# Kernel optimization log

Measured on AMD Instinct MI355X. Metric: run time of the kernel, lower is better.

## Reference

```python
import jax, jax.numpy as jnp
import numpy as np

KERNEL_MUL = 2.0
KERNEL_NUM = 5


def _mmd(source, target, kernel_mul=KERNEL_MUL, kernel_num=KERNEL_NUM, fix_sigma=None):
    n = source.shape[0]
    total = jnp.concatenate([source, target], axis=0)  # [2N, D]
    n_samples = total.shape[0]
    # Pairwise squared L2 distances via Gram matrix (same math as the
    # broadcasted (2N,2N,D) diff-square-sum, but O(N^2 D) GEMM instead).
    sq = jnp.sum(total * total, axis=1)                # [2N]
    gram = total @ total.T                             # [2N, 2N]
    L2 = sq[:, None] + sq[None, :] - 2.0 * gram        # [2N, 2N]
    if fix_sigma:
        bandwidth = fix_sigma
    else:
        # torch used L2_distance.data -> detached; match with stop_gradient
        bandwidth = jax.lax.stop_gradient(jnp.sum(L2)) / (n_samples ** 2 - n_samples)
    bandwidth = bandwidth / (kernel_mul ** (kernel_num // 2))
    kernels = jnp.zeros_like(L2)
    for i in range(kernel_num):
        kernels = kernels + jnp.exp(-L2 / (bandwidth * kernel_mul ** i))
    XX = kernels[:n, :n]
    YY = kernels[n:, n:]
    XY = kernels[:n, n:]
    YX = kernels[n:, :n]
    return jnp.mean(XX + YY - XY - YX)


def setup_inputs() -> dict:
    key = jax.random.key(0)
    k1, k2 = jax.random.split(key)
    N, D = 4096, 512
    source = jax.random.normal(k1, (N, D), dtype=jnp.float32)
    target = jax.random.normal(k2, (N, D), dtype=jnp.float32)
    return {"source": source, "target": target}


def reference(source, target):
    # MMD_sample_size = inf >= batch_size -> single full-batch MMD
    return _mmd(source, target)
```

## Files before the change

### kernel.cpp

```cpp
#include <hip/hip_runtime.h>
#include <hip/hip_fp16.h>


#define NS 8192
#define D_DIM 512
#define NTILE 64
#define NBLK 2080
#define PBLK 512

typedef _Float16 f16x8 __attribute__((ext_vector_type(8)));
typedef float f32x4 __attribute__((ext_vector_type(4)));

__global__ __launch_bounds__(256) void prep(const float* __restrict__ src,
                                            const float* __restrict__ tgt,
                                            __half* __restrict__ Th,
                                            float* __restrict__ sq,
                                            float* __restrict__ colp,
                                            float* __restrict__ sqp) {
    __shared__ float lcs[4][D_DIM];
    __shared__ float wsq[4];
    int tid = threadIdx.x, w = tid >> 6, l = tid & 63;
    int r0 = blockIdx.x * 16 + w * 4;
    float cs[8];
#pragma unroll
    for (int j = 0; j < 8; ++j) cs[j] = 0.f;
    float ws = 0.f;

#pragma unroll
    for (int rr = 0; rr < 4; ++rr) {
        int r = r0 + rr;
        const float* rowp = (r < 4096) ? (src + (size_t)r * D_DIM)
                                       : (tgt + (size_t)(r - 4096) * D_DIM);
        float4 v0 = *reinterpret_cast<const float4*>(rowp + l * 8);
        float4 v1 = *reinterpret_cast<const float4*>(rowp + l * 8 + 4);
        float f[8] = {v0.x, v0.y, v0.z, v0.w, v1.x, v1.y, v1.z, v1.w};
        __half h[8];
        float s = 0.f;
#pragma unroll
        for (int j = 0; j < 8; ++j) {
            h[j] = __float2half(f[j]);
            float fj = __half2float(h[j]);
            s += fj * fj;
            cs[j] += fj;
        }
        *reinterpret_cast<int4*>(Th + (size_t)r * D_DIM + l * 8) =
            *reinterpret_cast<const int4*>(h);
#pragma unroll
        for (int off = 32; off; off >>= 1) s += __shfl_xor(s, off, 64);
        if (l == 0) { sq[r] = s; ws += s; }
    }
    if (l == 0) wsq[w] = ws;
#pragma unroll
    for (int j = 0; j < 8; ++j) lcs[w][l * 8 + j] = cs[j];
    __syncthreads();
#pragma unroll
    for (int j = 0; j < 2; ++j) {
        int c = j * 256 + tid;
        colp[(size_t)blockIdx.x * D_DIM + c] =
            (lcs[0][c] + lcs[1][c]) + (lcs[2][c] + lcs[3][c]);
    }
    if (tid == 0) sqp[blockIdx.x] = (wsq[0] + wsq[1]) + (wsq[2] + wsq[3]);
}

__global__ __launch_bounds__(512) void combine(const float* __restrict__ colp,
                                               const float* __restrict__ sqp,
                                               float* __restrict__ Sacc,
                                               float* __restrict__ Cacc) {
    __shared__ float red[512];
    __shared__ float red2[512];
    int t = threadIdx.x;
    float s = 0.f;
#pragma unroll 16
    for (int b = 0; b < PBLK; ++b) s += colp[(size_t)b * D_DIM + t];
    float sv = sqp[t];
    red[t] = s * s; red2[t] = sv; __syncthreads();
    for (int off = 256; off; off >>= 1) {
        if (t < off) { red[t] += red[t + off]; red2[t] += red2[t + off]; }
        __syncthreads();
    }
    if (t == 0) { Cacc[0] = red[0]; Sacc[0] = red2[0]; }
}

__global__ __launch_bounds__(256, 2) void mmd_main(const __half* __restrict__ Th,
                                                   const float* __restrict__ sq,
                                                   const float* __restrict__ Sacc,
                                                   const float* __restrict__ Cacc,
                                                   float* __restrict__ partials) {
    __shared__ __half Ah[2][128 * 64];
    __shared__ __half Bh[2][128 * 64];
    __shared__ float wred[4];

    int borig = blockIdx.x;
    int b = (borig & 7) * (NBLK / 8) + (borig >> 3);
    int ti = 0, rem = b;
    while (rem >= NTILE - ti) { rem -= NTILE - ti; ++ti; }
    int tj = ti + rem;
    int ibase = ti * 128, jbase = tj * 128;
    float wgt = ((ti == tj) ? 1.f : 2.f) * (((ti < 32) == (tj < 32)) ? 1.f : -1.f);

    int tid = threadIdx.x;
    int wid = tid >> 6, lane = tid & 63;
    int wm = wid >> 1, wn = wid & 1;
    int cl = lane >> 4;

    double S = (double)Sacc[0];
    double C = (double)Cacc[0];

    f32x4 acc[4][4];
#pragma unroll
    for (int m = 0; m < 4; ++m)
#pragma unroll
        for (int n = 0; n < 4; ++n) acc[m][n] = f32x4{0.f, 0.f, 0.f, 0.f};

    auto STAGE = [&](int buf, int k0) {
#pragma unroll
        for (int it = 0; it < 4; ++it) {
            int h16 = tid + it * 256;
            int row = h16 >> 3, ch = h16 & 7;
            int scol = ((ch ^ (row & 7)) * 8);
            __builtin_amdgcn_global_load_lds(
                (const __attribute__((address_space(1))) unsigned int*)(Th + (size_t)(ibase + row) * D_DIM + k0 + scol),
                (__attribute__((address_space(3))) unsigned int*)(&Ah[buf][h16 * 8]), 16, 0, 0);
            __builtin_amdgcn_global_load_lds(
                (const __attribute__((address_space(1))) unsigned int*)(Th + (size_t)(jbase + row) * D_DIM + k0 + scol),
                (__attribute__((address_space(3))) unsigned int*)(&Bh[buf][h16 * 8]), 16, 0, 0);
        }
    };

    auto COMPUTE = [&](int buf) {
#pragma unroll
        for (int ks = 0; ks < 2; ++ks) {
            f16x8 afr[4], bfr[4];
#pragma unroll
            for (int m = 0; m < 4; ++m) {
                int ra = wm * 64 + m * 16 + (lane & 15);
                int pc = (ks * 4 + cl) ^ (ra & 7);
                afr[m] = *reinterpret_cast<const f16x8*>(&Ah[buf][ra * 64 + pc * 8]);
            }
#pragma unroll
            for (int n = 0; n < 4; ++n) {
                int rb = wn * 64 + n * 16 + (lane & 15);
                int pc = (ks * 4 + cl) ^ (rb & 7);
                bfr[n] = *reinterpret_cast<const f16x8*>(&Bh[buf][rb * 64 + pc * 8]);
            }
#pragma unroll
            for (int m = 0; m < 4; ++m)
#pragma unroll
                for (int n = 0; n < 4; ++n)
                    acc[m][n] = __builtin_amdgcn_mfma_f32_16x16x32_f16(afr[m], bfr[n], acc[m][n], 0, 0, 0);
        }
    };

    STAGE(0, 0);
    __syncthreads();
    int buf = 0;
#pragma unroll
    for (int t = 0; t < 7; ++t) {
        STAGE(buf ^ 1, (t + 1) * 64);
        COMPUTE(buf);
        __syncthreads();
        buf ^= 1;
    }
    COMPUTE(buf);

    double sumL2 = 2.0 * (double)NS * S - 2.0 * C;
    double bwv = sumL2 / ((double)NS * NS - (double)NS) / 4.0;
    float c0 = (float)(-1.4426950408889634 / bwv);
    float m2c0 = -2.f * c0;

    float sci[16], scj[4];
#pragma unroll
    for (int m = 0; m < 4; ++m)
#pragma unroll
        for (int r = 0; r < 4; ++r)
            sci[m * 4 + r] = sq[ibase + wm * 64 + m * 16 + (lane >> 4) * 4 + r] * c0;
#pragma unroll
    for (int n = 0; n < 4; ++n)
        scj[n] = sq[jbase + wn * 64 + n * 16 + (lane & 15)] * c0;

    float a0 = 0.f, a1 = 0.f, a2 = 0.f, a3 = 0.f, a4 = 0.f;
#pragma unroll
    for (int m = 0; m < 4; ++m)
#pragma unroll
        for (int n = 0; n < 4; ++n)
#pragma unroll
            for (int r = 0; r < 4; ++r) {
                float x0 = fmaf(acc[m][n][r], m2c0, sci[m * 4 + r] + scj[n]);
                float e0 = __builtin_amdgcn_exp2f(x0);
                float e1 = __builtin_amdgcn_sqrtf(e0);
                float e2 = __builtin_amdgcn_sqrtf(e1);
                float e3 = __builtin_amdgcn_sqrtf(e2);
                float e4 = __builtin_amdgcn_sqrtf(e3);
                a0 += e0; a1 += e1; a2 += e2; a3 += e3; a4 += e4;
            }
    float ksum = ((a0 + a1) + (a2 + a3)) + a4;
#pragma unroll
    for (int off = 32; off; off >>= 1) ksum += __shfl_xor(ksum, off, 64);
    if (lane == 0) wred[wid] = ksum;
    __syncthreads();
    if (tid == 0)
        partials[borig] = ((wred[0] + wred[1]) + (wred[2] + wred[3])) * wgt;
}

__global__ void finalize(const float* __restrict__ partials, float* __restrict__ out) {
    __shared__ double red[256];
    int t = threadIdx.x;
    double s = 0.0;
    for (int i = t; i < NBLK; i += 256) s += (double)partials[i];
    red[t] = s; __syncthreads();
    for (int off = 128; off; off >>= 1) { if (t < off) red[t] += red[t + off]; __syncthreads(); }
    if (t == 0) out[0] = (float)(red[0] * (1.0 / (4096.0 * 4096.0)));
}

extern "C" void kernel_launch(void* const* d_in, const int* in_sizes, int n_in,
                              void* d_out, int out_size, void* d_ws, size_t ws_size,
                              hipStream_t stream) {
    (void)in_sizes; (void)n_in; (void)out_size; (void)ws_size;
    const float* src = (const float*)d_in[0];
    const float* tgt = (const float*)d_in[1];
    char* ws = (char*)d_ws;
    __half* Th      = (__half*)ws;
    float* sq       = (float*)(ws + 8388608);
    float* colp     = (float*)(ws + 8421376);
    float* sqp      = (float*)(ws + 9469952);
    float* Sacc     = (float*)(ws + 9472000);
    float* Cacc     = (float*)(ws + 9472004);
    float* partials = (float*)(ws + 9472008);
    float* out      = (float*)d_out;

    hipLaunchKernelGGL(prep, dim3(PBLK), dim3(256), 0, stream, src, tgt, Th, sq, colp, sqp);
    hipLaunchKernelGGL(combine, dim3(1), dim3(512), 0, stream, colp, sqp, Sacc, Cacc);
    hipLaunchKernelGGL(mmd_main, dim3(NBLK), dim3(256), 0, stream, Th, sq, Sacc, Cacc, partials);
    hipLaunchKernelGGL(finalize, dim3(1), dim3(256), 0, stream, partials, out);
}
```

Measured before the change: 152.5 us.

## Use 8 waves per block and derive kernel sums by squaring one exp

```diff
diff --git a/kernel.cpp b/kernel.cpp
--- a/kernel.cpp
+++ b/kernel.cpp
@@ -81,14 +81,14 @@
     if (t == 0) { Cacc[0] = red[0]; Sacc[0] = red2[0]; }
 }
 
-__global__ __launch_bounds__(256, 2) void mmd_main(const __half* __restrict__ Th,
+__global__ __launch_bounds__(512, 4) void mmd_main(const __half* __restrict__ Th,
                                                    const float* __restrict__ sq,
                                                    const float* __restrict__ Sacc,
                                                    const float* __restrict__ Cacc,
                                                    float* __restrict__ partials) {
     __shared__ __half Ah[2][128 * 64];
     __shared__ __half Bh[2][128 * 64];
-    __shared__ float wred[4];
+    __shared__ float wred[8];
 
     int borig = blockIdx.x;
     int b = (borig & 7) * (NBLK / 8) + (borig >> 3);
@@ -100,22 +100,22 @@
 
     int tid = threadIdx.x;
     int wid = tid >> 6, lane = tid & 63;
-    int wm = wid >> 1, wn = wid & 1;
+    int wm = wid >> 2, wn = wid & 3;
     int cl = lane >> 4;
 
     double S = (double)Sacc[0];
     double C = (double)Cacc[0];
 
-    f32x4 acc[4][4];
+    f32x4 acc[4][2];
 #pragma unroll
     for (int m = 0; m < 4; ++m)
 #pragma unroll
-        for (int n = 0; n < 4; ++n) acc[m][n] = f32x4{0.f, 0.f, 0.f, 0.f};
+        for (int n = 0; n < 2; ++n) acc[m][n] = f32x4{0.f, 0.f, 0.f, 0.f};
 
     auto STAGE = [&](int buf, int k0) {
 #pragma unroll
-        for (int it = 0; it < 4; ++it) {
-            int h16 = tid + it * 256;
+        for (int it = 0; it < 2; ++it) {
+            int h16 = tid + it * 512;
             int row = h16 >> 3, ch = h16 & 7;
             int scol = ((ch ^ (row & 7)) * 8);
             __builtin_amdgcn_global_load_lds(
@@ -130,7 +130,7 @@
     auto COMPUTE = [&](int buf) {
 #pragma unroll
         for (int ks = 0; ks < 2; ++ks) {
-            f16x8 afr[4], bfr[4];
+            f16x8 afr[4], bfr[2];
 #pragma unroll
             for (int m = 0; m < 4; ++m) {
                 int ra = wm * 64 + m * 16 + (lane & 15);
@@ -138,15 +138,15 @@
                 afr[m] = *reinterpret_cast<const f16x8*>(&Ah[buf][ra * 64 + pc * 8]);
             }
 #pragma unroll
-            for (int n = 0; n < 4; ++n) {
-                int rb = wn * 64 + n * 16 + (lane & 15);
+            for (int n = 0; n < 2; ++n) {
+                int rb = wn * 32 + n * 16 + (lane & 15);
                 int pc = (ks * 4 + cl) ^ (rb & 7);
                 bfr[n] = *reinterpret_cast<const f16x8*>(&Bh[buf][rb * 64 + pc * 8]);
             }
 #pragma unroll
             for (int m = 0; m < 4; ++m)
 #pragma unroll
-                for (int n = 0; n < 4; ++n)
+                for (int n = 0; n < 2; ++n)
                     acc[m][n] = __builtin_amdgcn_mfma_f32_16x16x32_f16(afr[m], bfr[n], acc[m][n], 0, 0, 0);
         }
     };
@@ -165,41 +165,43 @@
 
     double sumL2 = 2.0 * (double)NS * S - 2.0 * C;
     double bwv = sumL2 / ((double)NS * NS - (double)NS) / 4.0;
-    float c0 = (float)(-1.4426950408889634 / bwv);
-    float m2c0 = -2.f * c0;
-
-    float sci[16], scj[4];
+    float c0s = (float)(-1.4426950408889634 / (bwv * 16.0));
+    float m2c0s = -2.f * c0s;
+
+    float sci[16], scj[2];
 #pragma unroll
     for (int m = 0; m < 4; ++m)
 #pragma unroll
         for (int r = 0; r < 4; ++r)
-            sci[m * 4 + r] = sq[ibase + wm * 64 + m * 16 + (lane >> 4) * 4 + r] * c0;
-#pragma unroll
-    for (int n = 0; n < 4; ++n)
-        scj[n] = sq[jbase + wn * 64 + n * 16 + (lane & 15)] * c0;
-
-    float a0 = 0.f, a1 = 0.f, a2 = 0.f, a3 = 0.f, a4 = 0.f;
+            sci[m * 4 + r] = sq[ibase + wm * 64 + m * 16 + (lane >> 4) * 4 + r] * c0s;
+#pragma unroll
+    for (int n = 0; n < 2; ++n)
+        scj[n] = sq[jbase + wn * 32 + n * 16 + (lane & 15)] * c0s;
+
+    float ksum = 0.f;
 #pragma unroll
     for (int m = 0; m < 4; ++m)
 #pragma unroll
-        for (int n = 0; n < 4; ++n)
+        for (int n = 0; n < 2; ++n)
 #pragma unroll
             for (int r = 0; r < 4; ++r) {
-                float x0 = fmaf(acc[m][n][r], m2c0, sci[m * 4 + r] + scj[n]);
-                float e0 = __builtin_amdgcn_exp2f(x0);
-                float e1 = __builtin_amdgcn_sqrtf(e0);
-                float e2 = __builtin_amdgcn_sqrtf(e1);
-                float e3 = __builtin_amdgcn_sqrtf(e2);
-                float e4 = __builtin_amdgcn_sqrtf(e3);
-                a0 += e0; a1 += e1; a2 += e2; a3 += e3; a4 += e4;
+                float x4 = fmaf(acc[m][n][r], m2c0s, sci[m * 4 + r] + scj[n]);
+                float e4 = __builtin_amdgcn_exp2f(x4);
+                float e3 = e4 * e4;
+                float e2 = e3 * e3;
+                float e1 = e2 * e2;
+                float e0 = e1 * e1;
+                ksum += ((e4 + e3) + (e2 + e1)) + e0;
             }
-    float ksum = ((a0 + a1) + (a2 + a3)) + a4;
 #pragma unroll
     for (int off = 32; off; off >>= 1) ksum += __shfl_xor(ksum, off, 64);
     if (lane == 0) wred[wid] = ksum;
     __syncthreads();
-    if (tid == 0)
-        partials[borig] = ((wred[0] + wred[1]) + (wred[2] + wred[3])) * wgt;
+    if (tid == 0) {
+        float tot = ((wred[0] + wred[1]) + (wred[2] + wred[3]))
+                  + ((wred[4] + wred[5]) + (wred[6] + wred[7]));
+        partials[borig] = tot * wgt;
+    }
 }
 
 __global__ void finalize(const float* __restrict__ partials, float* __restrict__ out) {
@@ -230,6 +232,6 @@
 
     hipLaunchKernelGGL(prep, dim3(PBLK), dim3(256), 0, stream, src, tgt, Th, sq, colp, sqp);
     hipLaunchKernelGGL(combine, dim3(1), dim3(512), 0, stream, colp, sqp, Sacc, Cacc);
-    hipLaunchKernelGGL(mmd_main, dim3(NBLK), dim3(256), 0, stream, Th, sq, Sacc, Cacc, partials);
+    hipLaunchKernelGGL(mmd_main, dim3(NBLK), dim3(512), 0, stream, Th, sq, Sacc, Cacc, partials);
     hipLaunchKernelGGL(finalize, dim3(1), dim3(256), 0, stream, partials, out);
 }
```

After: 147.2 us. 3.5% less time.
